# Performance work log

Hardware: AMD Instinct MI355X
Metric: run time of the kernel (lower is better)

Reference implementation:

```python
import jax, jax.numpy as jnp
import numpy as np

D_MODEL = 1024
NUM_HEADS = 16
HEAD_DIM = D_MODEL // NUM_HEADS  # used only for score scaling, as in the torch code


def setup_inputs() -> dict:
    key = jax.random.key(0)
    ks = jax.random.split(key, 8)
    B, S, D = 4, 2048, D_MODEL
    w_scale = 1.0 / np.sqrt(D)
    return {
        "x": jax.random.normal(ks[0], (B, S, D), dtype=jnp.float32),
        "Wq": jax.random.normal(ks[1], (D, D), dtype=jnp.float32) * w_scale,
        "bq": jnp.zeros((D,), dtype=jnp.float32),
        "Wk": jax.random.normal(ks[2], (D, D), dtype=jnp.float32) * w_scale,
        "bk": jnp.zeros((D,), dtype=jnp.float32),
        "Wv": jax.random.normal(ks[3], (D, D), dtype=jnp.float32) * w_scale,
        "bv": jnp.zeros((D,), dtype=jnp.float32),
        "temperature_scale": jnp.ones((1,), dtype=jnp.float32),
    }


def reference(x, Wq, bq, Wk, bk, Wv, bv, temperature_scale):
    # q, k, v: (B, S, D) -- no head split in the original module
    q = x @ Wq + bq
    k = x @ Wk + bk
    v = x @ Wv + bv
    scale = jnp.asarray(HEAD_DIM, x.dtype) ** 0.5
    # scores: (B, S, S)
    scores = jnp.einsum("bqd,bkd->bqk", q, k) / scale / temperature_scale[0]
    probs = jax.nn.softmax(scores, axis=-1)
    # per-row attention entropy (B, S, 1)
    entropy = -jnp.sum(probs * jnp.log(probs + 1e-8), axis=-1, keepdims=True)
    attention_output = jnp.einsum("bqk,bkd->bqd", probs, v)
    return attention_output, entropy.mean()
```

## Files before the change

kernel.cpp:

```cpp
#include <hip/hip_runtime.h>
#include <hip/hip_bf16.h>
#include <cstdint>
#include <cstddef>


typedef __attribute__((ext_vector_type(8))) short short8;
typedef __attribute__((ext_vector_type(4))) short short4v;
typedef __attribute__((ext_vector_type(4))) float f32x4;

#define GLOBAL_AS __attribute__((address_space(1)))
#define LDS_AS __attribute__((address_space(3)))

__device__ __forceinline__ void async_load16(const void* g, void* lds) {
  __builtin_amdgcn_global_load_lds((GLOBAL_AS void*)g, (LDS_AS void*)lds, 16, 0, 0);
}

__device__ __forceinline__ short f2bf_s(float x) {
  __hip_bfloat16 h = __float2bfloat16(x);
  return *reinterpret_cast<short*>(&h);
}

template <int MODE>
__device__ __forceinline__
void gemm_body(const __hip_bfloat16* __restrict__ A,
               const __hip_bfloat16* __restrict__ Bt,
               void* __restrict__ Cout,
               const float* __restrict__ bias,
               int K, int lda, int ldb, int ldc,
               __hip_bfloat16* __restrict__ sA,
               __hip_bfloat16* __restrict__ sB,
               int m0, int n0,
               const float* __restrict__ aux,
               float* __restrict__ stats) {
  const int tid  = threadIdx.x;
  const int lane = tid & 63;
  const int wid  = tid >> 6;
  const int wm = (wid >> 1) * 64;
  const int wn = (wid & 1) * 64;
  const int quad = lane >> 4;
  const int rc   = lane & 15;

  f32x4 acc[4][4] = {};

  const int srow = tid >> 3;
  const int scol = ((tid & 7) ^ ((tid >> 3) & 7)) * 8;
  const __hip_bfloat16* Ag = A  + (size_t)(m0 + srow) * lda + scol;
  const __hip_bfloat16* Bg = Bt + (size_t)(n0 + srow) * ldb + scol;

  for (int k0 = 0; k0 < K; k0 += 64) {
#pragma unroll
    for (int p = 0; p < 4; ++p) {
      async_load16(Ag + k0 + (size_t)(32 * p) * lda, &sA[(wid * 64 + 256 * p) * 8]);
      async_load16(Bg + k0 + (size_t)(32 * p) * ldb, &sB[(wid * 64 + 256 * p) * 8]);
    }
    __syncthreads();

#pragma unroll
    for (int kk = 0; kk < 2; ++kk) {
      const int xo = ((kk * 4 + quad) ^ (rc & 7)) * 8;
      short8 af[4], bf[4];
#pragma unroll
      for (int i = 0; i < 4; ++i)
        af[i] = *(const short8*)&sA[(wm + i * 16 + rc) * 64 + xo];
#pragma unroll
      for (int i = 0; i < 4; ++i)
        bf[i] = *(const short8*)&sB[(wn + i * 16 + rc) * 64 + xo];

#pragma unroll
      for (int mi = 0; mi < 4; ++mi)
#pragma unroll
        for (int ni = 0; ni < 4; ++ni)
          acc[mi][ni] = __builtin_amdgcn_mfma_f32_16x16x32_bf16(
              af[mi], bf[ni], acc[mi][ni], 0, 0, 0);
    }
    __syncthreads();
  }

  if (MODE == 3) {
    const int chunk = (n0 + wn) >> 6;
#pragma unroll
    for (int mi = 0; mi < 4; ++mi) {
      float l_acc[4] = {}, w_acc[4] = {};
#pragma unroll
      for (int ni = 0; ni < 4; ++ni)
#pragma unroll
        for (int r = 0; r < 4; ++r) {
          const float xv = acc[mi][ni][r];
          const float e = __expf(xv);
          acc[mi][ni][r] = e;
          l_acc[r] += e;
          w_acc[r] += e * xv;
        }
#pragma unroll
      for (int r = 0; r < 4; ++r) {
        float l = l_acc[r], w = w_acc[r];
#pragma unroll
        for (int off = 1; off < 16; off <<= 1) {
          l += __shfl_xor(l, off);
          w += __shfl_xor(w, off);
        }
        if (rc == 0) {
          const int row = m0 + wm + mi * 16 + quad * 4 + r;
          *(float2*)&stats[((size_t)row * 32 + chunk) * 2] = make_float2(l, w);
        }
      }
#pragma unroll
      for (int ni = 0; ni < 4; ++ni) {
        const int col = n0 + wn + ni * 16 + rc;
#pragma unroll
        for (int r = 0; r < 4; ++r) {
          const int row = m0 + wm + mi * 16 + quad * 4 + r;
          ((__hip_bfloat16*)Cout)[(size_t)row * ldc + col] =
              __float2bfloat16(acc[mi][ni][r]);
        }
      }
    }
  } else if (MODE == 4) {
#pragma unroll
    for (int mi = 0; mi < 4; ++mi) {
      float sc[4];
#pragma unroll
      for (int r = 0; r < 4; ++r)
        sc[r] = aux[m0 + wm + mi * 16 + quad * 4 + r];
#pragma unroll
      for (int ni = 0; ni < 4; ++ni) {
        const int col = n0 + wn + ni * 16 + rc;
#pragma unroll
        for (int r = 0; r < 4; ++r) {
          const int row = m0 + wm + mi * 16 + quad * 4 + r;
          ((float*)Cout)[(size_t)row * ldc + col] = acc[mi][ni][r] * sc[r];
        }
      }
    }
  } else {
    const float qsc = (MODE == 1 && aux) ? 1.0f / (8.0f * aux[0]) : 1.0f;
#pragma unroll
    for (int mi = 0; mi < 4; ++mi) {
#pragma unroll
      for (int ni = 0; ni < 4; ++ni) {
        const int col = n0 + wn + ni * 16 + rc;
        const float badd = bias[col];
        if (MODE == 2) {
          const int rowb = m0 + wm + mi * 16 + quad * 4;
          short4v o;
#pragma unroll
          for (int r = 0; r < 4; ++r) o[r] = f2bf_s(acc[mi][ni][r] + badd);
          const size_t idx = (size_t)(rowb >> 11) * (1024u * 2048u) +
                             (size_t)col * 2048u + (size_t)(rowb & 2047);
          *(short4v*)((short*)Cout + idx) = o;
        } else {
#pragma unroll
          for (int r = 0; r < 4; ++r) {
            const int row = m0 + wm + mi * 16 + quad * 4 + r;
            ((__hip_bfloat16*)Cout)[(size_t)row * ldc + col] =
                __float2bfloat16((acc[mi][ni][r] + badd) * qsc);
          }
        }
      }
    }
  }
}


__global__ __launch_bounds__(256)
void qkv_fused(const __hip_bfloat16* __restrict__ xb,
               const __hip_bfloat16* __restrict__ Wt,
               __hip_bfloat16* __restrict__ qb, __hip_bfloat16* __restrict__ kb,
               __hip_bfloat16* __restrict__ vt,
               const float* __restrict__ bq, const float* __restrict__ bk,
               const float* __restrict__ bv, const float* __restrict__ tptr) {
  __shared__ __align__(16) __hip_bfloat16 sA[128 * 64];
  __shared__ __align__(16) __hip_bfloat16 sB[128 * 64];
  const int lin = blockIdx.x;
  const int j = lin & 7, t = lin >> 3;
  const int x = t & 7;
  const int G = j + 8 * (t >> 3);
  const int z = G >> 6, y = G & 63;
  const int m0 = y * 128, n0 = x * 128;

  const __hip_bfloat16* B = Wt + (size_t)z * 1024 * 1024;
  if (z == 0)
    gemm_body<1>(xb, B, qb, bq, 1024, 1024, 1024, 1024, sA, sB, m0, n0, tptr, nullptr);
  else if (z == 1)
    gemm_body<1>(xb, B, kb, bk, 1024, 1024, 1024, 1024, sA, sB, m0, n0, nullptr, nullptr);
  else
    gemm_body<2>(xb, B, vt, bv, 1024, 1024, 1024, 0, sA, sB, m0, n0, nullptr, nullptr);
}

__global__ __launch_bounds__(256)
void scores_swz(const __hip_bfloat16* __restrict__ qb,
                const __hip_bfloat16* __restrict__ kb,
                __hip_bfloat16* __restrict__ Pt,
                float* __restrict__ stats) {
  __shared__ __align__(16) __hip_bfloat16 sA[128 * 64];
  __shared__ __align__(16) __hip_bfloat16 sB[128 * 64];
  const int lin = blockIdx.x;
  const int j = lin & 7, t = lin >> 3;
  const int w = t & 15;
  const int G = j + 8 * (t >> 4);
  const size_t z = G >> 4;
  const int r = G & 15;
  const int y = (r >> 2) * 4 + (w >> 2);
  const int x = (r & 3) * 4 + (w & 3);
  gemm_body<3>(qb + z * 2048 * 1024, kb + z * 2048 * 1024,
               Pt + z * 2048 * 2048, nullptr, 1024, 1024, 1024, 2048,
               sA, sB, y * 128, x * 128, nullptr, stats + z * 2048 * 64);
}

__global__ __launch_bounds__(256)
void pv_swz(const __hip_bfloat16* __restrict__ Pt,
            const __hip_bfloat16* __restrict__ vt,
            float* __restrict__ out,
            const float* __restrict__ inv_l) {
  __shared__ __align__(16) __hip_bfloat16 sA[128 * 64];
  __shared__ __align__(16) __hip_bfloat16 sB[128 * 64];
  const int lin = blockIdx.x;
  const int j = lin & 7, t = lin >> 3;
  const int w = t & 3;
  const int G = j + 8 * (t >> 2);
  const size_t z = G >> 5;
  const int r = G & 31;
  const int y = (r >> 2) * 2 + (w >> 1);
  const int x = (r & 3) * 2 + (w & 1);
  gemm_body<4>(Pt + z * 2048 * 2048, vt + z * 1024 * 2048,
               out + z * 2048 * 1024, nullptr, 2048, 2048, 2048, 1024,
               sA, sB, y * 128, x * 128, inv_l + z * 2048, nullptr);
}

__global__ __launch_bounds__(256)
void cast_f32_to_bf16(const float* __restrict__ src,
                      __hip_bfloat16* __restrict__ dst, int n) {
  const int i = (blockIdx.x * 256 + threadIdx.x) * 8;
  if (i >= n) return;
  const float4 a = *(const float4*)(src + i);
  const float4 b = *(const float4*)(src + i + 4);
  short8 o;
  o[0] = f2bf_s(a.x); o[1] = f2bf_s(a.y); o[2] = f2bf_s(a.z); o[3] = f2bf_s(a.w);
  o[4] = f2bf_s(b.x); o[5] = f2bf_s(b.y); o[6] = f2bf_s(b.z); o[7] = f2bf_s(b.w);
  *(short8*)((short*)dst + i) = o;
}

__global__ __launch_bounds__(256)
void transpose_cast_3w(const float* __restrict__ Wq, const float* __restrict__ Wk,
                       const float* __restrict__ Wv,
                       __hip_bfloat16* __restrict__ Wt) {
  __shared__ float tile[64][65];
  const int z = blockIdx.z;
  const float* src = (z == 0) ? Wq : (z == 1) ? Wk : Wv;
  __hip_bfloat16* dst = Wt + (size_t)z * 1024 * 1024;
  const int c0 = blockIdx.x * 64;
  const int r0 = blockIdx.y * 64;
  const int lane = threadIdx.x & 63;
  const int grp  = threadIdx.x >> 6;
#pragma unroll
  for (int i = 0; i < 16; ++i) {
    const int r = grp * 16 + i;
    tile[r][lane] = src[(size_t)(r0 + r) * 1024 + c0 + lane];
  }
  __syncthreads();
#pragma unroll
  for (int i = 0; i < 16; ++i) {
    const int r = grp * 16 + i;
    dst[(size_t)(c0 + r) * 1024 + r0 + lane] = __float2bfloat16(tile[lane][r]);
  }
}

__global__ __launch_bounds__(256)
void stats_reduce(const float* __restrict__ stats,
                  float* __restrict__ inv_l, float* __restrict__ Hrow) {
  const int row = blockIdx.x * 256 + threadIdx.x;
  const float* sp = stats + (size_t)row * 64;
  float l = 0.f, w = 0.f;
#pragma unroll
  for (int j = 0; j < 16; ++j) {
    const float4 a = *(const float4*)(sp + j * 4);
    l += a.x + a.z;
    w += a.y + a.w;
  }
  const float il = 1.0f / l;
  inv_l[row] = il;
  Hrow[row] = __logf(l) - w * il;
}

__global__ __launch_bounds__(256)
void reduce_entropy(const float* __restrict__ Hrow, float* __restrict__ out) {
  const int tid  = threadIdx.x;
  const int lane = tid & 63;
  const int wid  = tid >> 6;
  float s = 0.f;
#pragma unroll
  for (int j = 0; j < 8; ++j) {
    const float4 a = *(const float4*)(Hrow + j * 1024 + tid * 4);
    s += a.x + a.y + a.z + a.w;
  }
#pragma unroll
  for (int off = 1; off < 64; off <<= 1) s += __shfl_xor(s, off);
  __shared__ float red[4];
  if (lane == 0) red[wid] = s;
  __syncthreads();
  if (tid == 0)
    out[0] = (red[0] + red[1] + red[2] + red[3]) * (1.0f / 8192.0f);
}

extern "C" void kernel_launch(void* const* d_in, const int* in_sizes, int n_in,
                              void* d_out, int out_size, void* d_ws, size_t ws_size,
                              hipStream_t stream) {
  const float* x    = (const float*)d_in[0];
  const float* Wq   = (const float*)d_in[1];
  const float* bq   = (const float*)d_in[2];
  const float* Wk   = (const float*)d_in[3];
  const float* bk   = (const float*)d_in[4];
  const float* Wv   = (const float*)d_in[5];
  const float* bv   = (const float*)d_in[6];
  const float* temp = (const float*)d_in[7];
  float* out = (float*)d_out;
  char* ws = (char*)d_ws;

  __hip_bfloat16* qb    = (__hip_bfloat16*)(ws + 0);
  __hip_bfloat16* kb    = (__hip_bfloat16*)(ws + 16777216);
  __hip_bfloat16* vt    = (__hip_bfloat16*)(ws + 33554432);
  __hip_bfloat16* xb    = (__hip_bfloat16*)(ws + 50331648);
  __hip_bfloat16* Wt    = (__hip_bfloat16*)(ws + 67108864);
  __hip_bfloat16* Pt    = (__hip_bfloat16*)(ws + 73400320);
  float*          stats = (float*)(ws + 106954752);
  float*          inv_l = (float*)(ws + 109051904);
  float*          Hrow  = (float*)(ws + 109084672);

  cast_f32_to_bf16<<<4096, 256, 0, stream>>>(x, xb, 8388608);
  transpose_cast_3w<<<dim3(16, 16, 3), 256, 0, stream>>>(Wq, Wk, Wv, Wt);

  qkv_fused<<<1536, 256, 0, stream>>>(xb, Wt, qb, kb, vt, bq, bk, bv, temp);

  scores_swz<<<1024, 256, 0, stream>>>(qb, kb, Pt, stats);
  stats_reduce<<<32, 256, 0, stream>>>(stats, inv_l, Hrow);
  pv_swz<<<512, 256, 0, stream>>>(Pt, vt, out, inv_l);

  reduce_entropy<<<1, 256, 0, stream>>>(Hrow, out + 8388608);
}
```

Baseline: 250.2 us.

## Use 256x256-tile 8-wave pipelined GEMM for QKV projection and scores

Adds a 512-thread GEMM body that computes 256x256 output tiles. It uses an XOR-swizzled LDS layout, double-buffered async global-to-LDS loads issued between MFMA phases, and s_setprio around the MFMA groups. The QKV projection and the score/exp kernels now use it in place of the 128x128 version, which raises data reuse per loaded tile and cuts the block count. The cost is 128KB of dynamic LDS per block, which limits occupancy, and a 384-block QKV grid that may leave a partial wave of blocks at the end.

Result: slower. 256.3 us (+2.4%).

```diff
diff --git a/kernel.cpp b/kernel.cpp
--- a/kernel.cpp
+++ b/kernel.cpp
@@ -18,6 +18,257 @@
 __device__ __forceinline__ short f2bf_s(float x) {
   __hip_bfloat16 h = __float2bfloat16(x);
   return *reinterpret_cast<short*>(&h);
+}
+
+template <int MODE>
+__device__ __forceinline__
+void gemm256_body(const __hip_bfloat16* __restrict__ A,
+                  const __hip_bfloat16* __restrict__ Bt,
+                  void* __restrict__ Cout,
+                  const float* __restrict__ bias,
+                  int K, int lda, int ldb, int ldc,
+                  __hip_bfloat16* __restrict__ sA,
+                  __hip_bfloat16* __restrict__ sB,
+                  int m0, int n0,
+                  const float* __restrict__ aux,
+                  float* __restrict__ stats) {
+  const int tid  = threadIdx.x;
+  const int lane = tid & 63;
+  const int wid  = tid >> 6;
+  const int wm   = (wid >> 2) * 128;
+  const int wn   = (wid & 3) * 64;
+  const int quad = lane >> 4;
+  const int rc   = lane & 15;
+  const int rc7  = rc & 7;
+  const int wnr  = wn & 64;
+
+  f32x4 acc[8][4] = {};
+
+  const int r0   = tid >> 3;
+  const int scol = ((tid & 7) ^ (r0 & 7)) * 8;
+  const __hip_bfloat16* Ag = A  + (size_t)(m0 + r0) * lda + scol;
+  const __hip_bfloat16* Bg = Bt + (size_t)(n0 + r0) * ldb + scol;
+
+  const int NT = K >> 6;
+
+  auto stA = [&](int buf, int half, int kofs) {
+    const __hip_bfloat16* s = Ag + (size_t)(half * 128) * lda + kofs;
+    __hip_bfloat16* d = sA + (size_t)buf * 16384 + (size_t)half * 8192 + tid * 8;
+    async_load16(s, d);
+    async_load16(s + (size_t)64 * lda, d + 4096);
+  };
+  auto stB = [&](int buf, int half, int kofs) {
+    const __hip_bfloat16* s = Bg + (size_t)(half * 128) * ldb + kofs;
+    __hip_bfloat16* d = sB + (size_t)buf * 16384 + (size_t)half * 8192 + tid * 8;
+    async_load16(s, d);
+    async_load16(s + (size_t)64 * ldb, d + 4096);
+  };
+
+  const __hip_bfloat16* sAh0 = sA + (size_t)(wm >> 7) * 8192;
+  const __hip_bfloat16* sBh0 = sB + (size_t)(wn >> 7) * 8192;
+
+  {
+    const int k1 = (NT > 1 ? 1 : 0) * 64;
+    stA(0, 0, 0); stA(0, 1, 0); stB(0, 0, 0); stB(0, 1, 0);
+    stB(1, 0, k1); stB(1, 1, k1); stA(1, 0, k1);
+  }
+  asm volatile("s_waitcnt vmcnt(6)" ::: "memory");
+  __builtin_amdgcn_s_barrier();
+
+  for (int t = 0; t < NT; ++t) {
+    const int buf = t & 1;
+    const __hip_bfloat16* sAc = sAh0 + buf * 16384;
+    const __hip_bfloat16* sBc = sBh0 + buf * 16384;
+    const int k1 = ((t + 1 < NT) ? t + 1 : NT - 1) * 64;
+    const int k2 = ((t + 2 < NT) ? t + 2 : NT - 1) * 64;
+
+    short8 af[2][4], bfr[2][4], ah[2][4];
+
+#pragma unroll
+    for (int kk = 0; kk < 2; ++kk) {
+      const int gs = (kk * 4 + quad) ^ rc7;
+#pragma unroll
+      for (int i = 0; i < 4; ++i)
+        af[kk][i] = *(const short8*)&sAc[(i * 16 + rc) * 64 + gs * 8];
+#pragma unroll
+      for (int j = 0; j < 4; ++j)
+        bfr[kk][j] = *(const short8*)&sBc[(wnr + j * 16 + rc) * 64 + gs * 8];
+    }
+    stA(buf ^ 1, 1, k1);
+    __builtin_amdgcn_s_barrier();
+    __builtin_amdgcn_s_setprio(1);
+#pragma unroll
+    for (int mi = 0; mi < 4; ++mi)
+#pragma unroll
+      for (int ni = 0; ni < 2; ++ni)
+#pragma unroll
+        for (int kk = 0; kk < 2; ++kk)
+          acc[mi][ni] = __builtin_amdgcn_mfma_f32_16x16x32_bf16(
+              af[kk][mi], bfr[kk][ni], acc[mi][ni], 0, 0, 0);
+    __builtin_amdgcn_s_setprio(0);
+    __builtin_amdgcn_s_barrier();
+
+    __builtin_amdgcn_s_setprio(1);
+#pragma unroll
+    for (int mi = 0; mi < 4; ++mi)
+#pragma unroll
+      for (int ni = 2; ni < 4; ++ni)
+#pragma unroll
+        for (int kk = 0; kk < 2; ++kk)
+          acc[mi][ni] = __builtin_amdgcn_mfma_f32_16x16x32_bf16(
+              af[kk][mi], bfr[kk][ni], acc[mi][ni], 0, 0, 0);
+    __builtin_amdgcn_s_setprio(0);
+    __builtin_amdgcn_s_barrier();
+
+#pragma unroll
+    for (int kk = 0; kk < 2; ++kk) {
+      const int gs = (kk * 4 + quad) ^ rc7;
+#pragma unroll
+      for (int i = 0; i < 4; ++i)
+        ah[kk][i] = *(const short8*)&sAc[((i + 4) * 16 + rc) * 64 + gs * 8];
+    }
+    stB(buf, 0, k2);
+    __builtin_amdgcn_s_barrier();
+    __builtin_amdgcn_s_setprio(1);
+#pragma unroll
+    for (int mi = 0; mi < 4; ++mi)
+#pragma unroll
+      for (int ni = 0; ni < 2; ++ni)
+#pragma unroll
+        for (int kk = 0; kk < 2; ++kk)
+          acc[4 + mi][ni] = __builtin_amdgcn_mfma_f32_16x16x32_bf16(
+              ah[kk][mi], bfr[kk][ni], acc[4 + mi][ni], 0, 0, 0);
+    __builtin_amdgcn_s_setprio(0);
+    __builtin_amdgcn_s_barrier();
+
+    stB(buf, 1, k2);
+    stA(buf, 0, k2);
+    __builtin_amdgcn_s_barrier();
+    __builtin_amdgcn_s_setprio(1);
+#pragma unroll
+    for (int mi = 0; mi < 4; ++mi)
+#pragma unroll
+      for (int ni = 2; ni < 4; ++ni)
+#pragma unroll
+        for (int kk = 0; kk < 2; ++kk)
+          acc[4 + mi][ni] = __builtin_amdgcn_mfma_f32_16x16x32_bf16(
+              ah[kk][mi], bfr[kk][ni], acc[4 + mi][ni], 0, 0, 0);
+    __builtin_amdgcn_s_setprio(0);
+    asm volatile("s_waitcnt vmcnt(6)" ::: "memory");
+    __builtin_amdgcn_s_barrier();
+  }
+  asm volatile("s_waitcnt vmcnt(0)" ::: "memory");
+
+  if (MODE == 3) {
+    const int chunk = (n0 + wn) >> 6;
+#pragma unroll
+    for (int mi = 0; mi < 8; ++mi) {
+      float l_acc[4] = {}, w_acc[4] = {};
+#pragma unroll
+      for (int ni = 0; ni < 4; ++ni)
+#pragma unroll
+        for (int r = 0; r < 4; ++r) {
+          const float xv = acc[mi][ni][r];
+          const float e = __expf(xv);
+          acc[mi][ni][r] = e;
+          l_acc[r] += e;
+          w_acc[r] += e * xv;
+        }
+#pragma unroll
+      for (int r = 0; r < 4; ++r) {
+        float l = l_acc[r], w = w_acc[r];
+#pragma unroll
+        for (int off = 1; off < 16; off <<= 1) {
+          l += __shfl_xor(l, off);
+          w += __shfl_xor(w, off);
+        }
+        if (rc == 0) {
+          const int row = m0 + wm + mi * 16 + quad * 4 + r;
+          *(float2*)&stats[((size_t)row * 32 + chunk) * 2] = make_float2(l, w);
+        }
+      }
+#pragma unroll
+      for (int ni = 0; ni < 4; ++ni) {
+        const int col = n0 + wn + ni * 16 + rc;
+#pragma unroll
+        for (int r = 0; r < 4; ++r) {
+          const int row = m0 + wm + mi * 16 + quad * 4 + r;
+          ((__hip_bfloat16*)Cout)[(size_t)row * ldc + col] =
+              __float2bfloat16(acc[mi][ni][r]);
+        }
+      }
+    }
+  } else {
+    const float qsc = (MODE == 1 && aux) ? 1.0f / (8.0f * aux[0]) : 1.0f;
+#pragma unroll
+    for (int mi = 0; mi < 8; ++mi) {
+#pragma unroll
+      for (int ni = 0; ni < 4; ++ni) {
+        const int col = n0 + wn + ni * 16 + rc;
+        const float badd = bias[col];
+        if (MODE == 2) {
+          const int rowb = m0 + wm + mi * 16 + quad * 4;
+          short4v o;
+#pragma unroll
+          for (int r = 0; r < 4; ++r) o[r] = f2bf_s(acc[mi][ni][r] + badd);
+          const size_t idx = (size_t)(rowb >> 11) * (1024u * 2048u) +
+                             (size_t)col * 2048u + (size_t)(rowb & 2047);
+          *(short4v*)((short*)Cout + idx) = o;
+        } else {
+#pragma unroll
+          for (int r = 0; r < 4; ++r) {
+            const int row = m0 + wm + mi * 16 + quad * 4 + r;
+            ((__hip_bfloat16*)Cout)[(size_t)row * ldc + col] =
+                __float2bfloat16((acc[mi][ni][r] + badd) * qsc);
+          }
+        }
+      }
+    }
+  }
+}
+
+__global__ __launch_bounds__(512, 2)
+void qkv_fused256(const __hip_bfloat16* __restrict__ xb,
+                  const __hip_bfloat16* __restrict__ Wt,
+                  __hip_bfloat16* __restrict__ qb, __hip_bfloat16* __restrict__ kb,
+                  __hip_bfloat16* __restrict__ vt,
+                  const float* __restrict__ bq, const float* __restrict__ bk,
+                  const float* __restrict__ bv, const float* __restrict__ tptr) {
+  extern __shared__ __align__(16) __hip_bfloat16 smem[];
+  __hip_bfloat16* sA = smem;
+  __hip_bfloat16* sB = smem + 32768;
+  const int lin = blockIdx.x;
+  const int G  = (lin & 7) * 48 + (lin >> 3);
+  const int mt = G / 12, nt = G % 12;
+  const int m0  = mt * 256;
+  const int n0g = nt * 256;
+  const int z   = n0g >> 10;
+  const int n0  = n0g & 1023;
+  const __hip_bfloat16* B = Wt + (size_t)z * 1024 * 1024;
+  if (z == 0)
+    gemm256_body<1>(xb, B, qb, bq, 1024, 1024, 1024, 1024, sA, sB, m0, n0, tptr, nullptr);
+  else if (z == 1)
+    gemm256_body<1>(xb, B, kb, bk, 1024, 1024, 1024, 1024, sA, sB, m0, n0, nullptr, nullptr);
+  else
+    gemm256_body<2>(xb, B, vt, bv, 1024, 1024, 1024, 0, sA, sB, m0, n0, nullptr, nullptr);
+}
+
+__global__ __launch_bounds__(512, 2)
+void scores256(const __hip_bfloat16* __restrict__ qb,
+               const __hip_bfloat16* __restrict__ kb,
+               __hip_bfloat16* __restrict__ Pt,
+               float* __restrict__ stats) {
+  extern __shared__ __align__(16) __hip_bfloat16 smem[];
+  __hip_bfloat16* sA = smem;
+  __hip_bfloat16* sB = smem + 32768;
+  const int lin = blockIdx.x;
+  const int G = (lin & 7) * 32 + (lin >> 3);
+  const int z = G >> 6;
+  const int r = G & 63;
+  const int y = r >> 3, x = r & 7;
+  gemm256_body<3>(qb + (size_t)z * 2048 * 1024, kb + (size_t)z * 2048 * 1024,
+                  Pt + (size_t)z * 2048 * 2048, nullptr, 1024, 1024, 1024, 2048,
+                  sA, sB, y * 256, x * 256, nullptr, stats + (size_t)z * 2048 * 64);
 }
 
 template <int MODE>
@@ -76,46 +327,7 @@
     __syncthreads();
   }
 
-  if (MODE == 3) {
-    const int chunk = (n0 + wn) >> 6;
-#pragma unroll
-    for (int mi = 0; mi < 4; ++mi) {
-      float l_acc[4] = {}, w_acc[4] = {};
-#pragma unroll
-      for (int ni = 0; ni < 4; ++ni)
-#pragma unroll
-        for (int r = 0; r < 4; ++r) {
-          const float xv = acc[mi][ni][r];
-          const float e = __expf(xv);
-          acc[mi][ni][r] = e;
-          l_acc[r] += e;
-          w_acc[r] += e * xv;
-        }
-#pragma unroll
-      for (int r = 0; r < 4; ++r) {
-        float l = l_acc[r], w = w_acc[r];
-#pragma unroll
-        for (int off = 1; off < 16; off <<= 1) {
-          l += __shfl_xor(l, off);
-          w += __shfl_xor(w, off);
-        }
-        if (rc == 0) {
-          const int row = m0 + wm + mi * 16 + quad * 4 + r;
-          *(float2*)&stats[((size_t)row * 32 + chunk) * 2] = make_float2(l, w);
-        }
-      }
-#pragma unroll
-      for (int ni = 0; ni < 4; ++ni) {
-        const int col = n0 + wn + ni * 16 + rc;
-#pragma unroll
-        for (int r = 0; r < 4; ++r) {
-          const int row = m0 + wm + mi * 16 + quad * 4 + r;
-          ((__hip_bfloat16*)Cout)[(size_t)row * ldc + col] =
-              __float2bfloat16(acc[mi][ni][r]);
-        }
-      }
-    }
-  } else if (MODE == 4) {
+  if (MODE == 4) {
 #pragma unroll
     for (int mi = 0; mi < 4; ++mi) {
       float sc[4];
@@ -132,79 +344,7 @@
         }
       }
     }
-  } else {
-    const float qsc = (MODE == 1 && aux) ? 1.0f / (8.0f * aux[0]) : 1.0f;
-#pragma unroll
-    for (int mi = 0; mi < 4; ++mi) {
-#pragma unroll
-      for (int ni = 0; ni < 4; ++ni) {
-        const int col = n0 + wn + ni * 16 + rc;
-        const float badd = bias[col];
-        if (MODE == 2) {
-          const int rowb = m0 + wm + mi * 16 + quad * 4;
-          short4v o;
-#pragma unroll
-          for (int r = 0; r < 4; ++r) o[r] = f2bf_s(acc[mi][ni][r] + badd);
-          const size_t idx = (size_t)(rowb >> 11) * (1024u * 2048u) +
-                             (size_t)col * 2048u + (size_t)(rowb & 2047);
-          *(short4v*)((short*)Cout + idx) = o;
-        } else {
-#pragma unroll
-          for (int r = 0; r < 4; ++r) {
-            const int row = m0 + wm + mi * 16 + quad * 4 + r;
-            ((__hip_bfloat16*)Cout)[(size_t)row * ldc + col] =
-                __float2bfloat16((acc[mi][ni][r] + badd) * qsc);
-          }
-        }
-      }
-    }
-  }
-}
-
-
-__global__ __launch_bounds__(256)
-void qkv_fused(const __hip_bfloat16* __restrict__ xb,
-               const __hip_bfloat16* __restrict__ Wt,
-               __hip_bfloat16* __restrict__ qb, __hip_bfloat16* __restrict__ kb,
-               __hip_bfloat16* __restrict__ vt,
-               const float* __restrict__ bq, const float* __restrict__ bk,
-               const float* __restrict__ bv, const float* __restrict__ tptr) {
-  __shared__ __align__(16) __hip_bfloat16 sA[128 * 64];
-  __shared__ __align__(16) __hip_bfloat16 sB[128 * 64];
-  const int lin = blockIdx.x;
-  const int j = lin & 7, t = lin >> 3;
-  const int x = t & 7;
-  const int G = j + 8 * (t >> 3);
-  const int z = G >> 6, y = G & 63;
-  const int m0 = y * 128, n0 = x * 128;
-
-  const __hip_bfloat16* B = Wt + (size_t)z * 1024 * 1024;
-  if (z == 0)
-    gemm_body<1>(xb, B, qb, bq, 1024, 1024, 1024, 1024, sA, sB, m0, n0, tptr, nullptr);
-  else if (z == 1)
-    gemm_body<1>(xb, B, kb, bk, 1024, 1024, 1024, 1024, sA, sB, m0, n0, nullptr, nullptr);
-  else
-    gemm_body<2>(xb, B, vt, bv, 1024, 1024, 1024, 0, sA, sB, m0, n0, nullptr, nullptr);
-}
-
-__global__ __launch_bounds__(256)
-void scores_swz(const __hip_bfloat16* __restrict__ qb,
-                const __hip_bfloat16* __restrict__ kb,
-                __hip_bfloat16* __restrict__ Pt,
-                float* __restrict__ stats) {
-  __shared__ __align__(16) __hip_bfloat16 sA[128 * 64];
-  __shared__ __align__(16) __hip_bfloat16 sB[128 * 64];
-  const int lin = blockIdx.x;
-  const int j = lin & 7, t = lin >> 3;
-  const int w = t & 15;
-  const int G = j + 8 * (t >> 4);
-  const size_t z = G >> 4;
-  const int r = G & 15;
-  const int y = (r >> 2) * 4 + (w >> 2);
-  const int x = (r & 3) * 4 + (w & 3);
-  gemm_body<3>(qb + z * 2048 * 1024, kb + z * 2048 * 1024,
-               Pt + z * 2048 * 2048, nullptr, 1024, 1024, 1024, 2048,
-               sA, sB, y * 128, x * 128, nullptr, stats + z * 2048 * 64);
+  }
 }
 
 __global__ __launch_bounds__(256)
@@ -326,12 +466,21 @@
   float*          inv_l = (float*)(ws + 109051904);
   float*          Hrow  = (float*)(ws + 109084672);
 
+  static bool attr_done = false;
+  if (!attr_done) {
+    hipFuncSetAttribute((const void*)qkv_fused256,
+                        hipFuncAttributeMaxDynamicSharedMemorySize, 131072);
+    hipFuncSetAttribute((const void*)scores256,
+                        hipFuncAttributeMaxDynamicSharedMemorySize, 131072);
+    attr_done = true;
+  }
+
   cast_f32_to_bf16<<<4096, 256, 0, stream>>>(x, xb, 8388608);
   transpose_cast_3w<<<dim3(16, 16, 3), 256, 0, stream>>>(Wq, Wk, Wv, Wt);
 
-  qkv_fused<<<1536, 256, 0, stream>>>(xb, Wt, qb, kb, vt, bq, bk, bv, temp);
-
-  scores_swz<<<1024, 256, 0, stream>>>(qb, kb, Pt, stats);
+  qkv_fused256<<<384, 512, 131072, stream>>>(xb, Wt, qb, kb, vt, bq, bk, bv, temp);
+
+  scores256<<<256, 512, 131072, stream>>>(qb, kb, Pt, stats);
   stats_reduce<<<32, 256, 0, stream>>>(stats, inv_l, Hrow);
   pv_swz<<<512, 256, 0, stream>>>(Pt, vt, out, inv_l);
 
```
